# Optimization experiments

Measured on AMD Instinct MI355X. Metric: run time of the kernel, lower is better.

## Reference

```python
import jax, jax.numpy as jnp
import numpy as np

B, D, DFF, E, TOPK = 16384, 512, 2048, 8, 2


def setup_inputs() -> dict:
    key = jax.random.key(0)
    ks = jax.random.split(key, 5)
    scale_g = 1.0 / np.sqrt(D)
    scale_1 = 1.0 / np.sqrt(D)
    scale_2 = 1.0 / np.sqrt(DFF)
    return {
        "x": jax.random.normal(ks[0], (B, D), dtype=jnp.float32),
        "Wg": jax.random.normal(ks[1], (D, E), dtype=jnp.float32) * scale_g,
        "W1": jax.random.normal(ks[2], (E, D, DFF), dtype=jnp.float32) * scale_1,
        "b1": jnp.zeros((E, DFF), dtype=jnp.float32),
        "W2": jax.random.normal(ks[3], (E, DFF, D), dtype=jnp.float32) * scale_2,
        "b2": jnp.zeros((E, D), dtype=jnp.float32),
    }


def reference(x, Wg, W1, b1, W2, b2):
    # --- gate: top-k softmax routing weights, zeros elsewhere ---
    logits = x @ Wg                              # [B, E]
    probs = jax.nn.softmax(logits, axis=-1)      # [B, E]
    vals, idx = jax.lax.top_k(probs, TOPK)       # [B, K], [B, K]
    routing = jnp.zeros_like(probs).at[jnp.arange(x.shape[0])[:, None], idx].set(vals)  # [B, E]

    # --- experts: dense FFN per expert (equivalent math to masked dispatch) ---
    # original: gather selected tokens per expert, compute, scatter into
    # zeros[E, B, D], multiply by routing.T[:, :, None], sum over experts.
    # routing weight is exactly 0 for unselected tokens, so the dense form
    # out = sum_e routing[b, e] * expert_e(x_b) computes identical results.
    h = jax.nn.relu(jnp.einsum('bd,edf->ebf', x, W1) + b1[:, None, :])  # [E, B, DFF]
    y = jnp.einsum('ebf,efd->ebd', h, W2) + b2[:, None, :]              # [E, B, D]
    out = jnp.einsum('ebd,be->bd', y, routing)                          # [B, D]
    return out
```

## Files before the change

kernel.cpp:

```cpp
#include <hip/hip_runtime.h>
#include <stdint.h>

#define BTOK 16384
#define DM   512
#define DFF  2048
#define NE   8
#define NPAIR (BTOK*2)
#define MAXT 288
#define TPXMAX 36

typedef short s16x8 __attribute__((ext_vector_type(8)));
typedef float f32x4 __attribute__((ext_vector_type(4)));

__device__ __forceinline__ uint16_t f2b(float f) {
  uint32_t u = __float_as_uint(f);
  u += 0x7fff + ((u >> 16) & 1);
  return (uint16_t)(u >> 16);
}

__device__ __forceinline__ void g2l16(const void* gp, void* lp) {
  __builtin_amdgcn_global_load_lds(
      (__attribute__((address_space(1))) void*)(void*)gp,
      (__attribute__((address_space(3))) void*)lp, 16, 0, 0);
}

__global__ __launch_bounds__(256) void k_prep(
    const float* __restrict__ x, const float* __restrict__ wg,
    int* __restrict__ counts, int* __restrict__ tk_e, float* __restrict__ tk_w,
    uint16_t* __restrict__ xb,
    const float* __restrict__ w1, const float* __restrict__ w2,
    uint16_t* __restrict__ w1t, uint16_t* __restrict__ w2t) {
  __shared__ float t[32][33];
  __shared__ int hist[NE];
  int tid = threadIdx.x;

  if (blockIdx.x >= 256) {
    int fid = blockIdx.x - 256;
    int bx = fid & 1023, z = fid >> 10;
    int R, C, c0, r0;
    const float* src;
    uint16_t* dst;
    if (z < 8) { R = DM; C = DFF; c0 = (bx & 63) * 32; r0 = (bx >> 6) * 32;
                 src = w1 + (size_t)z * R * C; dst = w1t + (size_t)z * R * C; }
    else       { R = DFF; C = DM; c0 = (bx & 15) * 32; r0 = (bx >> 4) * 32;
                 src = w2 + (size_t)(z - 8) * R * C; dst = w2t + (size_t)(z - 8) * R * C; }
    int tx = tid & 31, ty = tid >> 5;
#pragma unroll
    for (int j = 0; j < 4; j++)
      t[ty + j * 8][tx] = src[(size_t)(r0 + ty + j * 8) * C + c0 + tx];
    __syncthreads();
    int oc = tid >> 3, ch = tid & 7;
    if (ch < 4) {
      uint16_t v[8];
#pragma unroll
      for (int k = 0; k < 8; k++) v[k] = f2b(t[ch * 8 + k][oc]);
      *(s16x8*)(dst + (size_t)(c0 + oc) * R + r0 + ch * 8) = *(s16x8*)v;
    }
    return;
  }

  int bid = blockIdx.x;
  int lane = tid & 63, wave = tid >> 6;
  if (tid < NE) hist[tid] = 0;
  __syncthreads();

  float wv[8][8];
#pragma unroll
  for (int j = 0; j < 8; j++) {
    const float4* wr = (const float4*)(wg + (size_t)(j * 64 + lane) * NE);
    float4 a = wr[0], b = wr[1];
    wv[j][0] = a.x; wv[j][1] = a.y; wv[j][2] = a.z; wv[j][3] = a.w;
    wv[j][4] = b.x; wv[j][5] = b.y; wv[j][6] = b.z; wv[j][7] = b.w;
  }

  int tok0 = bid * 64 + wave * 16;
  for (int tt = 0; tt < 16; tt++) {
    int tok = tok0 + tt;
    const float* xr = x + (size_t)tok * DM;
    float xv[8];
#pragma unroll
    for (int j = 0; j < 8; j++) xv[j] = xr[j * 64 + lane];
    float acc[NE];
#pragma unroll
    for (int e = 0; e < NE; e++) acc[e] = 0.f;
#pragma unroll
    for (int j = 0; j < 8; j++)
#pragma unroll
      for (int e = 0; e < NE; e++) acc[e] += xv[j] * wv[j][e];
#pragma unroll
    for (int e = 0; e < NE; e++) {
#pragma unroll
      for (int off = 32; off > 0; off >>= 1) acc[e] += __shfl_xor(acc[e], off, 64);
    }
    if (lane == 0) {
      float mx = acc[0];
      for (int e = 1; e < NE; e++) mx = fmaxf(mx, acc[e]);
      float p[NE], s = 0.f;
      for (int e = 0; e < NE; e++) { p[e] = __expf(acc[e] - mx); s += p[e]; }
      float inv = 1.f / s;
      int e0 = 0; float v0 = p[0];
      for (int e = 1; e < NE; e++) if (p[e] > v0) { v0 = p[e]; e0 = e; }
      int e1 = -1; float v1 = -1.f;
      for (int e = 0; e < NE; e++) if (e != e0 && p[e] > v1) { v1 = p[e]; e1 = e; }
      tk_e[tok * 2]     = e0; tk_w[tok * 2]     = v0 * inv;
      tk_e[tok * 2 + 1] = e1; tk_w[tok * 2 + 1] = v1 * inv;
      atomicAdd(&hist[e0], 1);
      atomicAdd(&hist[e1], 1);
    }
  }
  const float* xs = x + (size_t)bid * 32768;
  uint16_t* xd = xb + (size_t)bid * 32768;
#pragma unroll
  for (int i = 0; i < 16; i++) {
    int o = i * 2048 + tid * 8;
    float4 a = *(const float4*)(xs + o);
    float4 b = *(const float4*)(xs + o + 4);
    uint16_t v[8] = {f2b(a.x), f2b(a.y), f2b(a.z), f2b(a.w),
                     f2b(b.x), f2b(b.y), f2b(b.z), f2b(b.w)};
    *(s16x8*)(xd + o) = *(s16x8*)v;
  }
  __syncthreads();
  if (tid < NE) atomicAdd(&counts[tid], hist[tid]);
}

__global__ __launch_bounds__(256) void k_build(const int* __restrict__ tk_e, const float* __restrict__ tk_w,
                                               const int* __restrict__ counts, int* __restrict__ cursors,
                                               int* __restrict__ tok_of, int* __restrict__ pr_of,
                                               float* __restrict__ w_of,
                                               int* __restrict__ offsets,
                                               int* __restrict__ trB, int* __restrict__ texp,
                                               int* __restrict__ ntB) {
  __shared__ int lcnt[NE], lbase[NE], soff[NE + 1];
  int tid = threadIdx.x;
  int i = blockIdx.x * 256 + tid;
  if (tid < NE) {
    lcnt[tid] = 0;
    int off = 0;
    for (int e2 = 0; e2 < tid; e2++) off += counts[e2];
    soff[tid] = off;
  }
  __syncthreads();
  int e = tk_e[i];
  int local = atomicAdd(&lcnt[e], 1);
  __syncthreads();
  if (tid < NE) lbase[tid] = atomicAdd(&cursors[tid], lcnt[tid]);
  __syncthreads();
  int slot = soff[e] + lbase[e] + local;
  tok_of[slot] = i >> 1;
  pr_of[slot] = i;
  w_of[slot] = tk_w[i];

  if (blockIdx.x == 0) {
    if (tid < NE) {
      int base = 0;
#pragma unroll
      for (int e2 = 0; e2 < NE; e2++) if (e2 < tid) base += (counts[e2] + 127) >> 7;
      int o = soff[tid];
      int n = (counts[tid] + 127) >> 7;
      for (int k = 0; k < n; k++) { trB[base + k] = o + k * 128; texp[base + k] = tid; }
      offsets[tid] = o;
    }
    if (tid == 0) {
      int nt = 0, tot = 0;
#pragma unroll
      for (int e2 = 0; e2 < NE; e2++) { nt += (counts[e2] + 127) >> 7; tot += counts[e2]; }
      *ntB = nt;
      offsets[NE] = tot;
    }
  }
}


#define LDS16(off) (*(const s16x8*)((const char*)smem + (off)))
#define VM6 asm volatile("s_waitcnt vmcnt(6)" ::: "memory")
#define VM0 asm volatile("s_waitcnt vmcnt(0)" ::: "memory")
#define NOVM do{}while(0)
#define NOSTG do{}while(0)
#define MFMA16 __builtin_amdgcn_mfma_f32_16x16x32_bf16
#define BSTR 24576

#define DS0_P(bb) do{ \
  bf0 = LDS16(offB0 + (bb)*BSTR); bf1 = LDS16(offB1 + (bb)*BSTR); \
  bf2 = LDS16(offB2 + (bb)*BSTR); bf3 = LDS16(offB3 + (bb)*BSTR); \
  bf4 = LDS16(offB4 + (bb)*BSTR); bf5 = LDS16(offB5 + (bb)*BSTR); \
  bf6 = LDS16(offB6 + (bb)*BSTR); bf7 = LDS16(offB7 + (bb)*BSTR); \
  af0 = LDS16(offA0 + (bb)*BSTR); af1 = LDS16(offA1 + (bb)*BSTR); }while(0)
#define DS1_P(bb) do{ \
  af2 = LDS16(offA2 + (bb)*BSTR); af3 = LDS16(offA3 + (bb)*BSTR); }while(0)
#define SA_P(bb) do{ \
  g2l16(gA0, (char*)smem + (bb)*BSTR + wave*1024); \
  g2l16(gA1, (char*)smem + (bb)*BSTR + 4096 + wave*1024); \
  gA0 += 32; gA1 += 32; }while(0)
#define SB_P(bb) do{ \
  g2l16(gB0, (char*)smem + (bb)*BSTR + 8192 + wave*1024); \
  g2l16(gB1, (char*)smem + (bb)*BSTR + 12288 + wave*1024); \
  g2l16(gB2, (char*)smem + (bb)*BSTR + 16384 + wave*1024); \
  g2l16(gB3, (char*)smem + (bb)*BSTR + 20480 + wave*1024); \
  gB0 += 32; gB1 += 32; gB2 += 32; gB3 += 32; }while(0)
#define MM16A do{ \
  __builtin_amdgcn_s_setprio(1); \
  acc[0][0] = MFMA16(af0, bf0, acc[0][0], 0, 0, 0); \
  acc[1][0] = MFMA16(af1, bf0, acc[1][0], 0, 0, 0); \
  acc[0][1] = MFMA16(af0, bf1, acc[0][1], 0, 0, 0); \
  acc[1][1] = MFMA16(af1, bf1, acc[1][1], 0, 0, 0); \
  acc[0][2] = MFMA16(af0, bf2, acc[0][2], 0, 0, 0); \
  acc[1][2] = MFMA16(af1, bf2, acc[1][2], 0, 0, 0); \
  acc[0][3] = MFMA16(af0, bf3, acc[0][3], 0, 0, 0); \
  acc[1][3] = MFMA16(af1, bf3, acc[1][3], 0, 0, 0); \
  acc[0][4] = MFMA16(af0, bf4, acc[0][4], 0, 0, 0); \
  acc[1][4] = MFMA16(af1, bf4, acc[1][4], 0, 0, 0); \
  acc[0][5] = MFMA16(af0, bf5, acc[0][5], 0, 0, 0); \
  acc[1][5] = MFMA16(af1, bf5, acc[1][5], 0, 0, 0); \
  acc[0][6] = MFMA16(af0, bf6, acc[0][6], 0, 0, 0); \
  acc[1][6] = MFMA16(af1, bf6, acc[1][6], 0, 0, 0); \
  acc[0][7] = MFMA16(af0, bf7, acc[0][7], 0, 0, 0); \
  acc[1][7] = MFMA16(af1, bf7, acc[1][7], 0, 0, 0); \
  __builtin_amdgcn_s_setprio(0); }while(0)
#define MM16B do{ \
  __builtin_amdgcn_s_setprio(1); \
  acc[2][0] = MFMA16(af2, bf0, acc[2][0], 0, 0, 0); \
  acc[3][0] = MFMA16(af3, bf0, acc[3][0], 0, 0, 0); \
  acc[2][1] = MFMA16(af2, bf1, acc[2][1], 0, 0, 0); \
  acc[3][1] = MFMA16(af3, bf1, acc[3][1], 0, 0, 0); \
  acc[2][2] = MFMA16(af2, bf2, acc[2][2], 0, 0, 0); \
  acc[3][2] = MFMA16(af3, bf2, acc[3][2], 0, 0, 0); \
  acc[2][3] = MFMA16(af2, bf3, acc[2][3], 0, 0, 0); \
  acc[3][3] = MFMA16(af3, bf3, acc[3][3], 0, 0, 0); \
  acc[2][4] = MFMA16(af2, bf4, acc[2][4], 0, 0, 0); \
  acc[3][4] = MFMA16(af3, bf4, acc[3][4], 0, 0, 0); \
  acc[2][5] = MFMA16(af2, bf5, acc[2][5], 0, 0, 0); \
  acc[3][5] = MFMA16(af3, bf5, acc[3][5], 0, 0, 0); \
  acc[2][6] = MFMA16(af2, bf6, acc[2][6], 0, 0, 0); \
  acc[3][6] = MFMA16(af3, bf6, acc[3][6], 0, 0, 0); \
  acc[2][7] = MFMA16(af2, bf7, acc[2][7], 0, 0, 0); \
  acc[3][7] = MFMA16(af3, bf7, acc[3][7], 0, 0, 0); \
  __builtin_amdgcn_s_setprio(0); }while(0)
#define TILEP(bb, SA, SB, VMX) do{ \
  DS0_P(bb); SA; \
  __builtin_amdgcn_s_barrier(); \
  asm volatile("s_waitcnt lgkmcnt(0)" ::: "memory"); \
  MM16A; \
  __builtin_amdgcn_s_barrier(); \
  DS1_P(bb); SB; \
  __builtin_amdgcn_s_barrier(); \
  asm volatile("s_waitcnt lgkmcnt(0)" ::: "memory"); \
  MM16B; \
  VMX; \
  __builtin_amdgcn_s_barrier(); }while(0)

#define GEOM_SETUP \
  int tid = threadIdx.x, lane = tid & 63, wave = tid >> 6; \
  int wm = wave >> 1, wn = wave & 1; \
  int l15 = lane & 15, l4 = lane >> 4; \
  int offA0, offA1, offA2, offA3; \
  int offB0, offB1, offB2, offB3, offB4, offB5, offB6, offB7; \
  { int r; \
    r = wm*64 + 0*16 + l15; offA0 = r*64 + ((l4 ^ ((r>>1)&3)) << 4); \
    r = wm*64 + 1*16 + l15; offA1 = r*64 + ((l4 ^ ((r>>1)&3)) << 4); \
    r = wm*64 + 2*16 + l15; offA2 = r*64 + ((l4 ^ ((r>>1)&3)) << 4); \
    r = wm*64 + 3*16 + l15; offA3 = r*64 + ((l4 ^ ((r>>1)&3)) << 4); \
    r = wn*128 + 0*16 + l15; offB0 = 8192 + r*64 + ((l4 ^ ((r>>1)&3)) << 4); \
    r = wn*128 + 1*16 + l15; offB1 = 8192 + r*64 + ((l4 ^ ((r>>1)&3)) << 4); \
    r = wn*128 + 2*16 + l15; offB2 = 8192 + r*64 + ((l4 ^ ((r>>1)&3)) << 4); \
    r = wn*128 + 3*16 + l15; offB3 = 8192 + r*64 + ((l4 ^ ((r>>1)&3)) << 4); \
    r = wn*128 + 4*16 + l15; offB4 = 8192 + r*64 + ((l4 ^ ((r>>1)&3)) << 4); \
    r = wn*128 + 5*16 + l15; offB5 = 8192 + r*64 + ((l4 ^ ((r>>1)&3)) << 4); \
    r = wn*128 + 6*16 + l15; offB6 = 8192 + r*64 + ((l4 ^ ((r>>1)&3)) << 4); \
    r = wn*128 + 7*16 + l15; offB7 = 8192 + r*64 + ((l4 ^ ((r>>1)&3)) << 4); \
  } \
  int rp = tid >> 2, cp = (tid & 3) ^ ((rp >> 1) & 3);

#define ACC_INIT \
  f32x4 acc[4][8]; \
  _Pragma("unroll") for (int m = 0; m < 4; m++) \
  _Pragma("unroll") for (int n = 0; n < 8; n++) \
  _Pragma("unroll") for (int i = 0; i < 4; i++) acc[m][n][i] = 0.f; \
  s16x8 af0, af1, af2, af3, bf0, bf1, bf2, bf3, bf4, bf5, bf6, bf7;

__global__ __launch_bounds__(256, 2) void k_gemm1(
    const uint16_t* __restrict__ xb, const uint16_t* __restrict__ w1t,
    const float* __restrict__ b1,
    const int* __restrict__ tok_of, const int* __restrict__ offsets,
    const int* __restrict__ trB, const int* __restrict__ texp, const int* __restrict__ ntB,
    uint16_t* __restrict__ h) {
  __shared__ __align__(16) uint16_t smem[36864];
  int id = blockIdx.x;
  int nt = *ntB, tpx = (nt + 7) >> 3;
  int x = id & 7, q = id >> 3, j = q >> 3;
  if (j >= tpx) return;
  int tile = x * tpx + j;
  if (tile >= nt) return;
  int n0 = (q & 7) * 256;
  int e = texp[tile], row0 = trB[tile], end = offsets[e + 1];
  GEOM_SETUP;

  const uint16_t *gA0, *gA1, *gB0, *gB1, *gB2, *gB3;
  { int s0 = row0 + rp;      if (s0 >= end) s0 = end - 1;
    int s1 = row0 + rp + 64; if (s1 >= end) s1 = end - 1;
    gA0 = xb + (size_t)tok_of[s0] * DM + cp * 8;
    gA1 = xb + (size_t)tok_of[s1] * DM + cp * 8; }
  { const uint16_t* wb = w1t + (size_t)e * DFF * DM;
    gB0 = wb + (size_t)(n0 + rp +   0) * DM + cp * 8;
    gB1 = wb + (size_t)(n0 + rp +  64) * DM + cp * 8;
    gB2 = wb + (size_t)(n0 + rp + 128) * DM + cp * 8;
    gB3 = wb + (size_t)(n0 + rp + 192) * DM + cp * 8; }

  ACC_INIT;

  SA_P(0); SB_P(0); SA_P(1); SB_P(1);
  VM6;
  __builtin_amdgcn_s_barrier();

#pragma unroll 1
  for (int g = 0; g < 4; ++g) {
    TILEP(0, SA_P(2), SB_P(2), VM6);
    TILEP(1, SA_P(0), SB_P(0), VM6);
    TILEP(2, SA_P(1), SB_P(1), VM6);
  }
  TILEP(0, SA_P(2), SB_P(2), VM6);
  TILEP(1, SA_P(0), SB_P(0), VM6);
  TILEP(2, NOSTG, NOSTG, VM0);
  TILEP(0, NOSTG, NOSTG, NOVM);

  {
    float bv[8];
#pragma unroll
    for (int n = 0; n < 8; n++) bv[n] = b1[(size_t)e * DFF + n0 + wn * 128 + n * 16 + l15];
    char* wrg = (char*)smem + wave * 4608;
    int rr = lane >> 2, cb = lane & 3;
#pragma unroll
    for (int m = 0; m < 4; m++) {
#pragma unroll
      for (int n = 0; n < 8; n++)
#pragma unroll
        for (int i = 0; i < 4; i++) {
          float v = fmaxf(acc[m][n][i] + bv[n], 0.f);
          *(uint16_t*)(wrg + (l4 * 4 + i) * 272 + (n * 16 + l15) * 2) = f2b(v);
        }
      int gr = row0 + wm * 64 + m * 16 + rr;
      const char* src = wrg + rr * 272 + cb * 64;
      if (gr < end) {
        uint16_t* dst = h + (size_t)gr * DFF + n0 + wn * 128 + cb * 32;
        *(s16x8*)(dst +  0) = *(const s16x8*)(src +  0);
        *(s16x8*)(dst +  8) = *(const s16x8*)(src + 16);
        *(s16x8*)(dst + 16) = *(const s16x8*)(src + 32);
        *(s16x8*)(dst + 24) = *(const s16x8*)(src + 48);
      }
    }
  }
}

__global__ __launch_bounds__(256, 2) void k_gemm2(
    const uint16_t* __restrict__ h, const uint16_t* __restrict__ w2t,
    const float* __restrict__ b2, const float* __restrict__ w_of,
    const int* __restrict__ pr_of, const int* __restrict__ offsets,
    const int* __restrict__ trB, const int* __restrict__ texp, const int* __restrict__ ntB,
    float* __restrict__ y32) {
  __shared__ __align__(16) uint16_t smem[36864];
  int id = blockIdx.x;
  int nt = *ntB, tpx = (nt + 7) >> 3;
  int x = id & 7, q = id >> 3, j = q >> 1;
  if (j >= tpx) return;
  int tile = x * tpx + j;
  if (tile >= nt) return;
  int n0 = (q & 1) * 256;
  int e = texp[tile], row0 = trB[tile], end = offsets[e + 1];
  GEOM_SETUP;

  const uint16_t *gA0, *gA1, *gB0, *gB1, *gB2, *gB3;
  { int s0 = row0 + rp;      if (s0 >= end) s0 = end - 1;
    int s1 = row0 + rp + 64; if (s1 >= end) s1 = end - 1;
    gA0 = h + (size_t)s0 * DFF + cp * 8;
    gA1 = h + (size_t)s1 * DFF + cp * 8; }
  { const uint16_t* wb = w2t + (size_t)e * DM * DFF;
    gB0 = wb + (size_t)(n0 + rp +   0) * DFF + cp * 8;
    gB1 = wb + (size_t)(n0 + rp +  64) * DFF + cp * 8;
    gB2 = wb + (size_t)(n0 + rp + 128) * DFF + cp * 8;
    gB3 = wb + (size_t)(n0 + rp + 192) * DFF + cp * 8; }

  ACC_INIT;

  SA_P(0); SB_P(0); SA_P(1); SB_P(1);
  VM6;
  __builtin_amdgcn_s_barrier();

#pragma unroll 1
  for (int g = 0; g < 20; ++g) {
    TILEP(0, SA_P(2), SB_P(2), VM6);
    TILEP(1, SA_P(0), SB_P(0), VM6);
    TILEP(2, SA_P(1), SB_P(1), VM6);
  }
  TILEP(0, SA_P(2), SB_P(2), VM6);
  TILEP(1, SA_P(0), SB_P(0), VM6);
  TILEP(2, NOSTG, NOSTG, VM0);
  TILEP(0, NOSTG, NOSTG, NOVM);

  {
    float bv[8];
#pragma unroll
    for (int n = 0; n < 8; n++) bv[n] = b2[(size_t)e * DM + n0 + wn * 128 + n * 16 + l15];
#pragma unroll
    for (int m = 0; m < 4; m++)
#pragma unroll
      for (int i = 0; i < 4; i++) {
        int slot = row0 + wm * 64 + m * 16 + l4 * 4 + i;
        if (slot < end) {
          float wgt = w_of[slot];
          int pr = pr_of[slot];
          size_t base = (size_t)pr * DM + n0 + wn * 128 + l15;
#pragma unroll
          for (int n = 0; n < 8; n++) y32[base + n * 16] = wgt * (acc[m][n][i] + bv[n]);
        }
      }
  }
}

__global__ __launch_bounds__(256) void k_combine(const float* __restrict__ y32,
                                                 float* __restrict__ out) {
  int tid = threadIdx.x;
  int tok = blockIdx.x * 2 + (tid >> 7);
  int c4 = (tid & 127) * 4;
  const float4 a = *(const float4*)(y32 + (size_t)(tok * 2)     * DM + c4);
  const float4 b = *(const float4*)(y32 + (size_t)(tok * 2 + 1) * DM + c4);
  *(float4*)(out + (size_t)tok * DM + c4) = make_float4(a.x + b.x, a.y + b.y, a.z + b.z, a.w + b.w);
}

extern "C" void kernel_launch(void* const* d_in, const int* in_sizes, int n_in,
                              void* d_out, int out_size, void* d_ws, size_t ws_size,
                              hipStream_t stream) {
  const float* x  = (const float*)d_in[0];
  const float* wg = (const float*)d_in[1];
  const float* w1 = (const float*)d_in[2];
  const float* b1 = (const float*)d_in[3];
  const float* w2 = (const float*)d_in[4];
  const float* b2 = (const float*)d_in[5];
  float* out = (float*)d_out;

  char* ws = (char*)d_ws;
  const size_t MB = 1024 * 1024;
  uint16_t* xb   = (uint16_t*)ws;
  uint16_t* w1t  = (uint16_t*)(ws + 16 * MB);
  uint16_t* w2t  = (uint16_t*)(ws + 32 * MB);
  uint16_t* hbuf = (uint16_t*)(ws + 48 * MB);
  int* ctrl = (int*)(ws + 176 * MB);
  int*   counts  = ctrl;
  int*   cursors = ctrl + 8;
  int*   offsets = ctrl + 16;
  int*   ntB     = ctrl + 32;
  int*   trB     = ctrl + 64;
  int*   texp    = ctrl + 384;
  int*   tk_e    = ctrl + 1024;
  float* tk_w    = (float*)(ctrl + 1024 + 32768);
  int*   tok_of  = ctrl + 1024 + 2 * 32768;
  float* w_of    = (float*)(ctrl + 1024 + 3 * 32768);
  int*   pr_of   = ctrl + 1024 + 4 * 32768;
  float* y32     = (float*)(ws + 177 * MB);

  hipMemsetAsync(counts, 0, 16 * sizeof(int), stream);

  k_prep<<<256 + 16384, 256, 0, stream>>>(x, wg, counts, tk_e, tk_w, xb,
                                          w1, w2, w1t, w2t);
  k_build<<<NPAIR / 256, 256, 0, stream>>>(tk_e, tk_w, counts, cursors, tok_of, pr_of, w_of,
                                           offsets, trB, texp, ntB);
  k_gemm1<<<8 * TPXMAX * 8, 256, 0, stream>>>(xb, w1t, b1, tok_of, offsets,
                                              trB, texp, ntB, hbuf);
  k_gemm2<<<8 * TPXMAX * 2, 256, 0, stream>>>(hbuf, w2t, b2, w_of, pr_of, offsets,
                                              trB, texp, ntB, y32);
  k_combine<<<BTOK / 2, 256, 0, stream>>>(y32, out);
}
```

Baseline: 369.3 us.

## Switch GEMM pipelines from triple to double LDS buffering with fewer barriers

After: 1.126 ms. 3.05x slower.

```diff
diff --git a/kernel.cpp b/kernel.cpp
--- a/kernel.cpp
+++ b/kernel.cpp
@@ -187,16 +187,14 @@
   af0 = LDS16(offA0 + (bb)*BSTR); af1 = LDS16(offA1 + (bb)*BSTR); }while(0)
 #define DS1_P(bb) do{ \
   af2 = LDS16(offA2 + (bb)*BSTR); af3 = LDS16(offA3 + (bb)*BSTR); }while(0)
-#define SA_P(bb) do{ \
+#define SAB_P(bb) do{ \
   g2l16(gA0, (char*)smem + (bb)*BSTR + wave*1024); \
   g2l16(gA1, (char*)smem + (bb)*BSTR + 4096 + wave*1024); \
-  gA0 += 32; gA1 += 32; }while(0)
-#define SB_P(bb) do{ \
   g2l16(gB0, (char*)smem + (bb)*BSTR + 8192 + wave*1024); \
   g2l16(gB1, (char*)smem + (bb)*BSTR + 12288 + wave*1024); \
   g2l16(gB2, (char*)smem + (bb)*BSTR + 16384 + wave*1024); \
   g2l16(gB3, (char*)smem + (bb)*BSTR + 20480 + wave*1024); \
-  gB0 += 32; gB1 += 32; gB2 += 32; gB3 += 32; }while(0)
+  gA0 += 32; gA1 += 32; gB0 += 32; gB1 += 32; gB2 += 32; gB3 += 32; }while(0)
 #define MM16A do{ \
   __builtin_amdgcn_s_setprio(1); \
   acc[0][0] = MFMA16(af0, bf0, acc[0][0], 0, 0, 0); \
@@ -235,16 +233,12 @@
   acc[2][7] = MFMA16(af2, bf7, acc[2][7], 0, 0, 0); \
   acc[3][7] = MFMA16(af3, bf7, acc[3][7], 0, 0, 0); \
   __builtin_amdgcn_s_setprio(0); }while(0)
-#define TILEP(bb, SA, SB, VMX) do{ \
-  DS0_P(bb); SA; \
+#define TILE2(bb, STG, VMX) do{ \
+  DS0_P(bb); DS1_P(bb); \
+  asm volatile("s_waitcnt lgkmcnt(0)" ::: "memory"); \
   __builtin_amdgcn_s_barrier(); \
-  asm volatile("s_waitcnt lgkmcnt(0)" ::: "memory"); \
-  MM16A; \
-  __builtin_amdgcn_s_barrier(); \
-  DS1_P(bb); SB; \
-  __builtin_amdgcn_s_barrier(); \
-  asm volatile("s_waitcnt lgkmcnt(0)" ::: "memory"); \
-  MM16B; \
+  STG; \
+  MM16A; MM16B; \
   VMX; \
   __builtin_amdgcn_s_barrier(); }while(0)
 
@@ -277,13 +271,13 @@
   _Pragma("unroll") for (int i = 0; i < 4; i++) acc[m][n][i] = 0.f; \
   s16x8 af0, af1, af2, af3, bf0, bf1, bf2, bf3, bf4, bf5, bf6, bf7;
 
-__global__ __launch_bounds__(256, 2) void k_gemm1(
+__global__ __launch_bounds__(256, 3) void k_gemm1(
     const uint16_t* __restrict__ xb, const uint16_t* __restrict__ w1t,
     const float* __restrict__ b1,
     const int* __restrict__ tok_of, const int* __restrict__ offsets,
     const int* __restrict__ trB, const int* __restrict__ texp, const int* __restrict__ ntB,
     uint16_t* __restrict__ h) {
-  __shared__ __align__(16) uint16_t smem[36864];
+  __shared__ __align__(16) uint16_t smem[24576];
   int id = blockIdx.x;
   int nt = *ntB, tpx = (nt + 7) >> 3;
   int x = id & 7, q = id >> 3, j = q >> 3;
@@ -307,20 +301,17 @@
 
   ACC_INIT;
 
-  SA_P(0); SB_P(0); SA_P(1); SB_P(1);
+  SAB_P(0); SAB_P(1);
   VM6;
   __builtin_amdgcn_s_barrier();
 
 #pragma unroll 1
-  for (int g = 0; g < 4; ++g) {
-    TILEP(0, SA_P(2), SB_P(2), VM6);
-    TILEP(1, SA_P(0), SB_P(0), VM6);
-    TILEP(2, SA_P(1), SB_P(1), VM6);
-  }
-  TILEP(0, SA_P(2), SB_P(2), VM6);
-  TILEP(1, SA_P(0), SB_P(0), VM6);
-  TILEP(2, NOSTG, NOSTG, VM0);
-  TILEP(0, NOSTG, NOSTG, NOVM);
+  for (int g = 0; g < 7; ++g) {
+    TILE2(0, SAB_P(0), VM6);
+    TILE2(1, SAB_P(1), VM6);
+  }
+  TILE2(0, NOSTG, VM0);
+  TILE2(1, NOSTG, NOVM);
 
   {
     float bv[8];
@@ -350,13 +341,13 @@
   }
 }
 
-__global__ __launch_bounds__(256, 2) void k_gemm2(
+__global__ __launch_bounds__(256, 3) void k_gemm2(
     const uint16_t* __restrict__ h, const uint16_t* __restrict__ w2t,
     const float* __restrict__ b2, const float* __restrict__ w_of,
     const int* __restrict__ pr_of, const int* __restrict__ offsets,
     const int* __restrict__ trB, const int* __restrict__ texp, const int* __restrict__ ntB,
     float* __restrict__ y32) {
-  __shared__ __align__(16) uint16_t smem[36864];
+  __shared__ __align__(16) uint16_t smem[24576];
   int id = blockIdx.x;
   int nt = *ntB, tpx = (nt + 7) >> 3;
   int x = id & 7, q = id >> 3, j = q >> 1;
@@ -380,20 +371,17 @@
 
   ACC_INIT;
 
-  SA_P(0); SB_P(0); SA_P(1); SB_P(1);
+  SAB_P(0); SAB_P(1);
   VM6;
   __builtin_amdgcn_s_barrier();
 
 #pragma unroll 1
-  for (int g = 0; g < 20; ++g) {
-    TILEP(0, SA_P(2), SB_P(2), VM6);
-    TILEP(1, SA_P(0), SB_P(0), VM6);
-    TILEP(2, SA_P(1), SB_P(1), VM6);
-  }
-  TILEP(0, SA_P(2), SB_P(2), VM6);
-  TILEP(1, SA_P(0), SB_P(0), VM6);
-  TILEP(2, NOSTG, NOSTG, VM0);
-  TILEP(0, NOSTG, NOSTG, NOVM);
+  for (int g = 0; g < 31; ++g) {
+    TILE2(0, SAB_P(0), VM6);
+    TILE2(1, SAB_P(1), VM6);
+  }
+  TILE2(0, NOSTG, VM0);
+  TILE2(1, NOSTG, NOVM);
 
   {
     float bv[8];
```
